# Optimization experiments

Hardware: AMD Instinct MI355X
Metric: run time of the kernel (lower is better)

## Reference

```python
import jax, jax.numpy as jnp
import numpy as np

EPS = 1e-10

def _iou(a, b):
    """IoU for boxes in (cx, cy, w, h) format; a, b: (..., 4)."""
    a_min = a[..., :2] - a[..., 2:] * 0.5
    a_max = a[..., :2] + a[..., 2:] * 0.5
    b_min = b[..., :2] - b[..., 2:] * 0.5
    b_max = b[..., :2] + b[..., 2:] * 0.5
    inter_wh = jnp.clip(jnp.minimum(a_max, b_max) - jnp.maximum(a_min, b_min), 0.0)
    inter = inter_wh[..., 0] * inter_wh[..., 1]
    area_a = a[..., 2] * a[..., 3]
    area_b = b[..., 2] * b[..., 3]
    return inter / (area_a + area_b - inter + EPS)

def setup_inputs() -> dict:
    key = jax.random.key(0)
    k1, k2, k3 = jax.random.split(key, 3)
    BATCH, S, C = 16384, 7, 30
    # uniform in (0.01, 1) so sqrt() of w,h channels is finite/differentiable
    preds = jax.random.uniform(k1, (BATCH, S, S, C), jnp.float32, 0.01, 1.0)
    labels = jax.random.uniform(k2, (BATCH, S, S, C), jnp.float32, 0.01, 1.0)
    obj = jax.random.bernoulli(k3, 0.15, (BATCH, S, S)).astype(jnp.float32)
    labels = labels.at[..., 4].set(obj)  # code branches on labels[...,4] == 1
    return {"preds": preds, "labels": labels}

def reference(preds, labels):
    batch = preds.shape[0]
    obj = labels[..., 4] == 1.0  # (B, S, S)
    # faithful quirk: label bbox x-coord is read transposed (labels[i, y, x, 0])
    lb0 = jnp.swapaxes(labels[..., 0], 1, 2)
    lbox = jnp.stack([lb0, labels[..., 1], labels[..., 2], labels[..., 3]], axis=-1)
    iou1 = _iou(preds[..., 0:4], lbox)
    iou2 = _iou(preds[..., 5:9], lbox)
    choose1 = iou1 > iou2
    # branch where box 1 is responsible
    b1 = (5.0 * jnp.sum((preds[..., 0:2] - labels[..., 0:2]) ** 2, -1)
          + jnp.sum((jnp.sqrt(preds[..., 2:4]) - jnp.sqrt(labels[..., 2:4])) ** 2, -1)
          + (iou1 - preds[..., 4]) ** 2
          + 0.5 * preds[..., 9] ** 2)
    # branch where box 2 is responsible (targets read from labels[...,5:9] as in source)
    b2 = (5.0 * jnp.sum((preds[..., 5:7] - labels[..., 5:7]) ** 2, -1)
          + jnp.sum((jnp.sqrt(preds[..., 7:9]) - jnp.sqrt(labels[..., 7:9])) ** 2, -1)
          + (iou2 - preds[..., 9]) ** 2
          + 0.5 * preds[..., 4] ** 2)
    cls = jnp.sum((labels[..., 10:] - preds[..., 10:]) ** 2, -1)
    obj_loss = jnp.where(choose1, b1, b2) + cls
    noobj_loss = 0.5 * (preds[..., 4] ** 2 + preds[..., 9] ** 2)
    total = jnp.sum(jnp.where(obj, obj_loss, noobj_loss))
    return total / batch
```

## Files before the change

### kernel.cpp

```cpp
#include <hip/hip_runtime.h>


#define BATCH 16384
#define S 7
#define C 30
#define NCELLS (BATCH * S * S)
#define BLOCK 256
#define CELLS_PER_BLOCK 256
#define NBLK (NCELLS / CELLS_PER_BLOCK)

#define SP_BASE 8192
#define LDS_FLOATS (8192 + 4 * 1920)

#define GLOBAL_LOAD_LDS16(g, l)                                         \
    __builtin_amdgcn_global_load_lds(                                   \
        (const __attribute__((address_space(1))) void*)(g),             \
        (__attribute__((address_space(3))) void*)(l), 16, 0, 0)

__device__ __forceinline__ float sq(float v) { return v * v; }

__device__ __forceinline__ float iou_box(float acx, float acy, float aw, float ah,
                                         float bcx, float bcy, float bw, float bh) {
    float ax0 = acx - aw * 0.5f, ax1 = acx + aw * 0.5f;
    float ay0 = acy - ah * 0.5f, ay1 = acy + ah * 0.5f;
    float bx0 = bcx - bw * 0.5f, bx1 = bcx + bw * 0.5f;
    float by0 = bcy - bh * 0.5f, by1 = bcy + bh * 0.5f;
    float iw = fmaxf(fminf(ax1, bx1) - fmaxf(ax0, bx0), 0.0f);
    float ih = fmaxf(fminf(ay1, by1) - fmaxf(ay0, by0), 0.0f);
    float inter = iw * ih;
    float denom = aw * ah + bw * bh - inter + 1e-10f;
    return inter / denom;
}

__global__ __launch_bounds__(BLOCK) void yolo_partial_kernel(
        const float* __restrict__ preds,
        const float* __restrict__ labels,
        float* __restrict__ partials) {
    __shared__ __align__(16) float lds[LDS_FLOATS];
    __shared__ float wsum[4];

    const int tid  = threadIdx.x;
    const int lane = tid & 63;
    const int wv   = tid >> 6;
    const int cell0 = blockIdx.x * CELLS_PER_BLOCK + wv * 64;

    const float4* gp = reinterpret_cast<const float4*>(preds  + (size_t)cell0 * C);
    const float4* gl = reinterpret_cast<const float4*>(labels + (size_t)cell0 * C);
    float* sl = &lds[wv * 2048];
    float* sp = &lds[SP_BASE + wv * 1920];

    #pragma unroll
    for (int k = 0; k < 7; ++k)
        GLOBAL_LOAD_LDS16(gl + k * 64 + lane, (char*)sl + (size_t)k * 1024);
    #pragma unroll
    for (int k = 0; k < 7; ++k)
        GLOBAL_LOAD_LDS16(gp + k * 64 + lane, (char*)sp + (size_t)k * 1024);
    {
        const float4* src = (lane < 32) ? (gl + 448 + lane) : (gp + 448 + (lane - 32));
        GLOBAL_LOAD_LDS16(src, (char*)sl + 7168);
    }

    const int cell = cell0 + lane;
    const int b    = cell / (S * S);
    const int rem  = cell - b * (S * S);
    const int y    = rem / S;
    const int x    = rem - y * S;
    const int pc   = b * (S * S) + x * S + y;
    const float lb0 = labels[(size_t)pc * C];

    asm volatile("s_waitcnt vmcnt(0)" ::: "memory");
    __builtin_amdgcn_sched_barrier(0);

    {
        float2 v = *reinterpret_cast<const float2*>(&sl[1920 + 2 * lane]);
        *reinterpret_cast<float2*>(&sp[1792 + 2 * lane]) = v;
    }

    const float* p = sp + lane * C;
    const float* l = sl + lane * C;
    float pv[C], lv[C];
    #pragma unroll
    for (int i = 0; i < C / 2; ++i) {
        float2 tp = *reinterpret_cast<const float2*>(p + 2 * i);
        pv[2 * i] = tp.x; pv[2 * i + 1] = tp.y;
        float2 tl = *reinterpret_cast<const float2*>(l + 2 * i);
        lv[2 * i] = tl.x; lv[2 * i + 1] = tl.y;
    }

    float iou1 = iou_box(pv[0], pv[1], pv[2], pv[3], lb0, lv[1], lv[2], lv[3]);
    float iou2 = iou_box(pv[5], pv[6], pv[7], pv[8], lb0, lv[1], lv[2], lv[3]);

    float b1 = 5.0f * (sq(pv[0] - lv[0]) + sq(pv[1] - lv[1]))
             + sq(sqrtf(pv[2]) - sqrtf(lv[2])) + sq(sqrtf(pv[3]) - sqrtf(lv[3]))
             + sq(iou1 - pv[4])
             + 0.5f * pv[9] * pv[9];

    float b2 = 5.0f * (sq(pv[5] - lv[5]) + sq(pv[6] - lv[6]))
             + sq(sqrtf(pv[7]) - sqrtf(lv[7])) + sq(sqrtf(pv[8]) - sqrtf(lv[8]))
             + sq(iou2 - pv[9])
             + 0.5f * pv[4] * pv[4];

    float cls = 0.0f;
    #pragma unroll
    for (int c = 10; c < C; ++c) cls += sq(lv[c] - pv[c]);

    float obj_loss   = ((iou1 > iou2) ? b1 : b2) + cls;
    float noobj_loss = 0.5f * (pv[4] * pv[4] + pv[9] * pv[9]);
    float loss = (lv[4] == 1.0f) ? obj_loss : noobj_loss;

    #pragma unroll
    for (int off = 32; off > 0; off >>= 1)
        loss += __shfl_down(loss, off, 64);

    if (lane == 0) wsum[wv] = loss;
    __syncthreads();
    if (tid == 0) {
        partials[blockIdx.x] = wsum[0] + wsum[1] + wsum[2] + wsum[3];
    }
}

__global__ __launch_bounds__(256) void yolo_reduce_kernel(
        const float* __restrict__ partials,
        float* __restrict__ out) {
    const int tid = threadIdx.x;
    float s = 0.0f;
    for (int i = tid; i < NBLK; i += 256) s += partials[i];

    #pragma unroll
    for (int off = 32; off > 0; off >>= 1)
        s += __shfl_down(s, off, 64);

    __shared__ float wsum[4];
    int lane = tid & 63;
    int wv   = tid >> 6;
    if (lane == 0) wsum[wv] = s;
    __syncthreads();
    if (tid == 0) {
        out[0] = (wsum[0] + wsum[1] + wsum[2] + wsum[3]) * (1.0f / (float)BATCH);
    }
}

extern "C" void kernel_launch(void* const* d_in, const int* in_sizes, int n_in,
                              void* d_out, int out_size, void* d_ws, size_t ws_size,
                              hipStream_t stream) {
    const float* preds  = (const float*)d_in[0];
    const float* labels = (const float*)d_in[1];
    float* out = (float*)d_out;
    float* partials = (float*)d_ws;

    yolo_partial_kernel<<<NBLK, BLOCK, 0, stream>>>(preds, labels, partials);
    yolo_reduce_kernel<<<1, 256, 0, stream>>>(partials, out);
}
```

Before: 205.4 us.

## Persistent single-wave blocks with double-buffered LDS tile prefetch

Replaces one 256-thread block per 256 cells with 1280 persistent 64-thread blocks. Each block loops over 8 or 12 wave-sized tiles and double-buffers them in LDS, issuing the global-to-LDS loads for the next tile before computing the current one. The aim is to overlap memory latency with compute and cut block launch overhead. The trade-off is fewer waves in flight, so latency hiding now depends on the manual vmcnt waits, and those waits are tied to an exact count of outstanding loads.

```diff
diff --git a/kernel.cpp b/kernel.cpp
--- a/kernel.cpp
+++ b/kernel.cpp
@@ -5,17 +5,23 @@
 #define S 7
 #define C 30
 #define NCELLS (BATCH * S * S)
-#define BLOCK 256
-#define CELLS_PER_BLOCK 256
-#define NBLK (NCELLS / CELLS_PER_BLOCK)
+#define NBLK 3136
+#define NW 1280
 
-#define SP_BASE 8192
-#define LDS_FLOATS (8192 + 4 * 1920)
+#define BUF_FLOATS 3968
+#define SP_OFF 2048
 
 #define GLOBAL_LOAD_LDS16(g, l)                                         \
     __builtin_amdgcn_global_load_lds(                                   \
         (const __attribute__((address_space(1))) void*)(g),             \
         (__attribute__((address_space(3))) void*)(l), 16, 0, 0)
+
+#define WAIT_VMCNT16()                                                  \
+    do { asm volatile("s_waitcnt vmcnt(16)" ::: "memory");              \
+         __builtin_amdgcn_sched_barrier(0); } while (0)
+#define WAIT_VMCNT0()                                                   \
+    do { asm volatile("s_waitcnt vmcnt(0)" ::: "memory");               \
+         __builtin_amdgcn_sched_barrier(0); } while (0)
 
 __device__ __forceinline__ float sq(float v) { return v * v; }
 
@@ -32,52 +38,43 @@
     return inter / denom;
 }
 
-__global__ __launch_bounds__(BLOCK) void yolo_partial_kernel(
-        const float* __restrict__ preds,
-        const float* __restrict__ labels,
-        float* __restrict__ partials) {
-    __shared__ __align__(16) float lds[LDS_FLOATS];
-    __shared__ float wsum[4];
-
-    const int tid  = threadIdx.x;
-    const int lane = tid & 63;
-    const int wv   = tid >> 6;
-    const int cell0 = blockIdx.x * CELLS_PER_BLOCK + wv * 64;
-
-    const float4* gp = reinterpret_cast<const float4*>(preds  + (size_t)cell0 * C);
-    const float4* gl = reinterpret_cast<const float4*>(labels + (size_t)cell0 * C);
-    float* sl = &lds[wv * 2048];
-    float* sp = &lds[SP_BASE + wv * 1920];
-
+__device__ __forceinline__ void stage_tile(const float* __restrict__ preds,
+                                           const float* __restrict__ labels,
+                                           int base_cell, float* bf, int lane) {
+    const float4* gp = reinterpret_cast<const float4*>(preds  + (size_t)base_cell * C);
+    const float4* gl = reinterpret_cast<const float4*>(labels + (size_t)base_cell * C);
     #pragma unroll
     for (int k = 0; k < 7; ++k)
-        GLOBAL_LOAD_LDS16(gl + k * 64 + lane, (char*)sl + (size_t)k * 1024);
+        GLOBAL_LOAD_LDS16(gl + k * 64 + lane, (char*)bf + (size_t)k * 1024);
     #pragma unroll
     for (int k = 0; k < 7; ++k)
-        GLOBAL_LOAD_LDS16(gp + k * 64 + lane, (char*)sp + (size_t)k * 1024);
-    {
-        const float4* src = (lane < 32) ? (gl + 448 + lane) : (gp + 448 + (lane - 32));
-        GLOBAL_LOAD_LDS16(src, (char*)sl + 7168);
-    }
+        GLOBAL_LOAD_LDS16(gp + k * 64 + lane,
+                          (char*)bf + (size_t)SP_OFF * 4 + (size_t)k * 1024);
+    const float4* src = (lane < 32) ? (gl + 448 + lane) : (gp + 448 + (lane - 32));
+    GLOBAL_LOAD_LDS16(src, (char*)bf + 7168);
+}
 
-    const int cell = cell0 + lane;
+__device__ __forceinline__ float issue_lb0(const float* __restrict__ labels,
+                                           int base_cell, int lane) {
+    const int cell = base_cell + lane;
     const int b    = cell / (S * S);
     const int rem  = cell - b * (S * S);
     const int y    = rem / S;
     const int x    = rem - y * S;
     const int pc   = b * (S * S) + x * S + y;
-    const float lb0 = labels[(size_t)pc * C];
+    const float* a = labels + (size_t)pc * C;
+    float lb;
+    asm volatile("global_load_dword %0, %1, off" : "=&v"(lb) : "v"(a) : "memory");
+    return lb;
+}
 
-    asm volatile("s_waitcnt vmcnt(0)" ::: "memory");
-    __builtin_amdgcn_sched_barrier(0);
-
+__device__ __forceinline__ float compute_tile(float* bf, float lb0, int lane) {
     {
-        float2 v = *reinterpret_cast<const float2*>(&sl[1920 + 2 * lane]);
-        *reinterpret_cast<float2*>(&sp[1792 + 2 * lane]) = v;
+        float2 v = *reinterpret_cast<const float2*>(&bf[1920 + 2 * lane]);
+        *reinterpret_cast<float2*>(&bf[SP_OFF + 1792 + 2 * lane]) = v;
     }
-
-    const float* p = sp + lane * C;
-    const float* l = sl + lane * C;
+    const float* p = &bf[SP_OFF + lane * C];
+    const float* l = &bf[lane * C];
     float pv[C], lv[C];
     #pragma unroll
     for (int i = 0; i < C / 2; ++i) {
@@ -111,12 +108,57 @@
     #pragma unroll
     for (int off = 32; off > 0; off >>= 1)
         loss += __shfl_down(loss, off, 64);
+    return loss;
+}
 
-    if (lane == 0) wsum[wv] = loss;
-    __syncthreads();
-    if (tid == 0) {
-        partials[blockIdx.x] = wsum[0] + wsum[1] + wsum[2] + wsum[3];
+__global__ __launch_bounds__(64) void yolo_partial_kernel(
+        const float* __restrict__ preds,
+        const float* __restrict__ labels,
+        float* __restrict__ partials) {
+    __shared__ __align__(16) float lds[2 * BUF_FLOATS];
+
+    const int lane = threadIdx.x;
+    const int gid  = blockIdx.x;
+    const int ngrp  = (gid < 576) ? 3 : 2;
+    const int total = 4 * ngrp;
+
+    float* bufA = lds;
+    float* bufB = lds + BUF_FLOATS;
+
+    #define TILE_BASE(seq) ((gid + ((seq) >> 2) * NW) * 256 + ((seq) & 3) * 64)
+
+    stage_tile(preds, labels, TILE_BASE(0), bufA, lane);
+    float lbA = issue_lb0(labels, TILE_BASE(0), lane);
+    float lbB = 0.0f;
+
+    float gsum = 0.0f;
+    int grp_out = gid;
+
+    for (int s = 0; s < total; s += 2) {
+        stage_tile(preds, labels, TILE_BASE(s + 1), bufB, lane);
+        lbB = issue_lb0(labels, TILE_BASE(s + 1), lane);
+        WAIT_VMCNT16();
+        {
+            float w = compute_tile(bufA, lbA, lane);
+            gsum = ((s & 3) == 0) ? w : gsum + w;
+        }
+        if (s + 2 < total) {
+            stage_tile(preds, labels, TILE_BASE(s + 2), bufA, lane);
+            lbA = issue_lb0(labels, TILE_BASE(s + 2), lane);
+            WAIT_VMCNT16();
+        } else {
+            WAIT_VMCNT0();
+        }
+        {
+            float w = compute_tile(bufB, lbB, lane);
+            gsum = gsum + w;
+            if (((s + 1) & 3) == 3) {
+                if (lane == 0) partials[grp_out] = gsum;
+                grp_out += NW;
+            }
+        }
     }
+    #undef TILE_BASE
 }
 
 __global__ __launch_bounds__(256) void yolo_reduce_kernel(
@@ -148,6 +190,6 @@
     float* out = (float*)d_out;
     float* partials = (float*)d_ws;
 
-    yolo_partial_kernel<<<NBLK, BLOCK, 0, stream>>>(preds, labels, partials);
+    yolo_partial_kernel<<<NW, 64, 0, stream>>>(preds, labels, partials);
     yolo_reduce_kernel<<<1, 256, 0, stream>>>(partials, out);
 }
```

Result: slower. 214.9 us (+4.6%).
